# Kernel tuning notes

Hardware: AMD Instinct MI355X
Metric: run time of the kernel (lower is better)

The kernel has to match this reference:

```python
import jax, jax.numpy as jnp
import numpy as np

N = 4096
F_IN = 512
F_OUT = 64
H = 8
ALPHA = 0.2
NEG_BIG = -9e15


def setup_inputs() -> dict:
    key = jax.random.key(0)
    ks = jax.random.split(key, 7)
    h = jax.random.normal(ks[0], (N, F_IN), dtype=jnp.float32)
    mask = jax.random.randint(ks[1], (N, N), 0, 2, dtype=jnp.int32)
    # per-head linear W: weight [H, F_IN, F_OUT], bias [H, F_OUT] (xavier-ish scale)
    w_scale = 1.414 * np.sqrt(6.0 / (F_IN + F_OUT))
    W = jax.random.uniform(ks[2], (H, F_IN, F_OUT), dtype=jnp.float32, minval=-w_scale, maxval=w_scale)
    bW = jnp.zeros((H, F_OUT), dtype=jnp.float32)
    # attention linear A: [2*F_OUT, 1] split into a_l (acts on Wh_i) and a_r (acts on Wh_j)
    a_scale = 1.414 * np.sqrt(6.0 / (2 * F_OUT + 1))
    a_l = jax.random.uniform(ks[3], (H, F_OUT), dtype=jnp.float32, minval=-a_scale, maxval=a_scale)
    a_r = jax.random.uniform(ks[4], (H, F_OUT), dtype=jnp.float32, minval=-a_scale, maxval=a_scale)
    bA = jnp.zeros((H,), dtype=jnp.float32)
    return {"h": h, "mask": mask, "W": W, "bW": bW, "a_l": a_l, "a_r": a_r, "bA": bA}


def reference(h, mask, W, bW, a_l, a_r, bA):
    # Wh: [H, N, F_OUT]
    Wh = jnp.einsum('ni,hio->hno', h, W) + bW[:, None, :]
    # A([Wh_i ; Wh_j]) decomposed as outer sum: e[h,i,j] = a_l.Wh_i + a_r.Wh_j + bA
    el = jnp.einsum('hno,ho->hn', Wh, a_l)  # [H, N]
    er = jnp.einsum('hno,ho->hn', Wh, a_r)  # [H, N]
    e = el[:, :, None] + er[:, None, :] + bA[:, None, None]  # [H, N, N]
    e = jax.nn.leaky_relu(e, negative_slope=ALPHA)
    e = jnp.where(mask[None] > 0, e, NEG_BIG)
    a = jax.nn.softmax(e, axis=-1)  # softmax over neighbors j (dim=1 in torch)
    # dropout omitted (eval mode / deterministic reference)
    aWh = jnp.einsum('hij,hjo->hio', a, Wh)  # [H, N, F_OUT]
    out = jax.nn.elu(aWh)  # last=False
    # concat heads along feature dim -> [N, H*F_OUT]
    return jnp.transpose(out, (1, 0, 2)).reshape(N, H * F_OUT)
```

## Files before the change

### kernel.cpp

```cpp
#include <hip/hip_runtime.h>
#include <hip/hip_bf16.h>
#include <hip/hip_fp16.h>

#define NN 4096
#define FIN 512
#define FOUT 64
#define NH 8
#define ALPHA 0.2f
#define PSCALE 4096.0f

typedef unsigned int uint;
typedef unsigned short ushort;
typedef unsigned char uchar;
typedef unsigned long long ull;
typedef __attribute__((ext_vector_type(8))) short short8;
typedef __attribute__((ext_vector_type(8))) _Float16 half8;
typedef __attribute__((ext_vector_type(4))) float floatx4;
typedef __attribute__((ext_vector_type(4))) uint uintx4;
typedef __attribute__((ext_vector_type(2))) uint uintx2;

__device__ __forceinline__ float bf2f(ushort s) { return __uint_as_float(((uint)s) << 16); }
__device__ __forceinline__ ushort f2bf(float f) {
    uint u = __float_as_uint(f);
    u += 0x7fffu + ((u >> 16) & 1u);
    return (ushort)(u >> 16);
}
__device__ __forceinline__ ushort f2h(float f) {
    return __half_as_ushort(__float2half_rn(f));
}

__device__ __forceinline__ int detect_bf16(const ushort* __restrict__ hraw) {
    int lane = threadIdx.x & 63;
    float a = fabsf(bf2f(hraw[2 * lane]));
    ull bal = __ballot(a >= 1e-3f && a <= 100.0f);
    return __popcll(bal) >= 32;
}

#define PM_BLKS 8192
#define CV_BLKS 1024
#define TW_BLKS 32

__global__ __launch_bounds__(256) void prep_kernel(
    const int* __restrict__ mask, uchar* __restrict__ mb,
    const void* __restrict__ hraw, ushort* __restrict__ bh,
    const void* __restrict__ Wraw, ushort* __restrict__ WT)
{
    const int b = blockIdx.x, t = threadIdx.x;
    if (b < PM_BLKS) {
        size_t gid = (size_t)b * 256 + t;
        const int* p = mask + gid * 8;
        int4 aa = *(const int4*)p;
        int4 bb = *(const int4*)(p + 4);
        uint by = (uint)(aa.x > 0)        | ((uint)(aa.y > 0) << 1)
                | ((uint)(aa.z > 0) << 2) | ((uint)(aa.w > 0) << 3)
                | ((uint)(bb.x > 0) << 4) | ((uint)(bb.y > 0) << 5)
                | ((uint)(bb.z > 0) << 6) | ((uint)(bb.w > 0) << 7);
        mb[gid] = (uchar)by;
    } else if (b < PM_BLKS + CV_BLKS) {
        int isbf = detect_bf16((const ushort*)hraw);
        size_t e0 = ((size_t)(b - PM_BLKS) * 256 + t) * 8;
        if (isbf) {
            *(uint4*)(bh + e0) = *(const uint4*)((const ushort*)hraw + e0);
        } else {
            const float* s = (const float*)hraw + e0;
            float4 f0 = *(const float4*)s;
            float4 f1 = *(const float4*)(s + 4);
            uint4 o;
            o.x = (uint)f2bf(f0.x) | ((uint)f2bf(f0.y) << 16);
            o.y = (uint)f2bf(f0.z) | ((uint)f2bf(f0.w) << 16);
            o.z = (uint)f2bf(f1.x) | ((uint)f2bf(f1.y) << 16);
            o.w = (uint)f2bf(f1.z) | ((uint)f2bf(f1.w) << 16);
            *(uint4*)(bh + e0) = o;
        }
    } else {
        int isbf = detect_bf16((const ushort*)hraw);
        int b2 = b - PM_BLKS - CV_BLKS;
        int h = b2 >> 2, kq = b2 & 3;
        int o = t & 63, sub = t >> 6;
        int kbase = kq * 128 + sub * 32;
        uint pk[16];
#pragma unroll
        for (int kk = 0; kk < 32; kk += 2) {
            float v0, v1;
            size_t s0 = ((size_t)h * FIN + kbase + kk) * FOUT + o;
            size_t s1 = s0 + FOUT;
            if (isbf) { v0 = bf2f(((const ushort*)Wraw)[s0]); v1 = bf2f(((const ushort*)Wraw)[s1]); }
            else      { v0 = ((const float*)Wraw)[s0];        v1 = ((const float*)Wraw)[s1]; }
            pk[kk >> 1] = (uint)f2bf(v0) | ((uint)f2bf(v1) << 16);
        }
        ushort* dst = WT + ((size_t)h * FOUT + o) * FIN + kbase;
#pragma unroll
        for (int q = 0; q < 4; q++)
            *(uint4*)(dst + q * 8) = make_uint4(pk[q*4], pk[q*4+1], pk[q*4+2], pk[q*4+3]);
    }
}

__global__ __launch_bounds__(256) void khv_kernel(const float* __restrict__ er,
                                                  float* __restrict__ Kh,
                                                  ushort* __restrict__ vt,
                                                  ushort* __restrict__ zt) {
    __shared__ float red[256];
    int h = blockIdx.x >> 3, sl = blockIdx.x & 7, t = threadIdx.x;
    float m = -3.0e38f;
    for (int j = t; j < NN; j += 256) m = fmaxf(m, er[(size_t)h * NN + j]);
    red[t] = m;
    __syncthreads();
    for (int s = 128; s >= 1; s >>= 1) {
        if (t < s) red[t] = fmaxf(red[t], red[t + s]);
        __syncthreads();
    }
    float kh = red[0];
    if (t == 0 && sl == 0) Kh[h] = kh;
    int j = sl * 512 + t;
#pragma unroll
    for (int q = 0; q < 2; q++, j += 256) {
        float d = er[(size_t)h * NN + j] - kh;
        vt[(size_t)h * NN + j] = f2h(__expf(d));
        zt[(size_t)h * NN + j] = f2h(__expf(ALPHA * d));
    }
}

__global__ __launch_bounds__(256) void wh_kernel(
    const ushort* __restrict__ hmat, const ushort* __restrict__ WT,
    const void* __restrict__ bWr, const void* __restrict__ alr,
    const void* __restrict__ arr, const void* __restrict__ bAr,
    const ushort* __restrict__ hraw,
    ushort* __restrict__ WhT, float* __restrict__ el, float* __restrict__ er)
{
    __shared__ __align__(16) ushort sT[64][72];
    const int t = threadIdx.x, lane = t & 63, wid = t >> 6;
    const int head = blockIdx.y, rbase = blockIdx.x * 64;
    const int lm = lane & 15, lq = lane >> 4;

    floatx4 C[4];
#pragma unroll
    for (int cg = 0; cg < 4; cg++) C[cg] = (floatx4){0.f, 0.f, 0.f, 0.f};

    const ushort* Ap = hmat + (size_t)(rbase + wid * 16 + lm) * FIN + lq * 8;
    const ushort* Bp = WT + (size_t)head * FOUT * FIN + (size_t)lm * FIN + lq * 8;

#pragma unroll
    for (int kc = 0; kc < 16; kc++) {
        short8 a = *(const short8*)(Ap + kc * 32);
#pragma unroll
        for (int cg = 0; cg < 4; cg++) {
            short8 b = *(const short8*)(Bp + (size_t)cg * 16 * FIN + kc * 32);
            C[cg] = __builtin_amdgcn_mfma_f32_16x16x32_bf16(a, b, C[cg], 0, 0, 0);
        }
    }

    const int isbf = detect_bf16(hraw);
    float bA = isbf ? bf2f(((const ushort*)bAr)[head]) : ((const float*)bAr)[head];
    float pel[4] = {0.f, 0.f, 0.f, 0.f}, per[4] = {0.f, 0.f, 0.f, 0.f};
#pragma unroll
    for (int cg = 0; cg < 4; cg++) {
        int o = head * FOUT + cg * 16 + lm;
        float bw = isbf ? bf2f(((const ushort*)bWr)[o]) : ((const float*)bWr)[o];
        float av = isbf ? bf2f(((const ushort*)alr)[o]) : ((const float*)alr)[o];
        float rv = isbf ? bf2f(((const ushort*)arr)[o]) : ((const float*)arr)[o];
        ushort pk[4];
#pragma unroll
        for (int r = 0; r < 4; r++) {
            float v = C[cg][r] + bw;
            pel[r] += v * av;
            per[r] += v * rv;
            pk[r] = f2h(v);
        }
        ushort4 p4; p4.x = pk[0]; p4.y = pk[1]; p4.z = pk[2]; p4.w = pk[3];
        *(ushort4*)(&sT[cg * 16 + lm][wid * 16 + lq * 4]) = p4;
    }
#pragma unroll
    for (int off = 1; off < 16; off <<= 1) {
#pragma unroll
        for (int r = 0; r < 4; r++) {
            pel[r] += __shfl_xor(pel[r], off);
            per[r] += __shfl_xor(per[r], off);
        }
    }
    if (lm == 0) {
#pragma unroll
        for (int r = 0; r < 4; r++) {
            int row = rbase + wid * 16 + lq * 4 + r;
            el[(size_t)head * NN + row] = pel[r];
            er[(size_t)head * NN + row] = per[r] + bA;
        }
    }
    __syncthreads();
    {
        int o = t >> 2, ch = t & 3;
        uint4 v0 = *(const uint4*)(&sT[o][ch * 16]);
        uint4 v1 = *(const uint4*)(&sT[o][ch * 16 + 8]);
        ushort* d = WhT + ((size_t)head * FOUT + o) * NN + rbase + ch * 16;
        *(uint4*)d = v0;
        *(uint4*)(d + 8) = v1;
    }
}

__device__ __forceinline__ uint pkmul(uint a, uint b) {
    uint d; asm("v_pk_mul_f16 %0,%1,%2" : "=v"(d) : "v"(a), "v"(b)); return d;
}
__device__ __forceinline__ uint pkmax(uint a, uint b) {
    uint d; asm("v_pk_max_f16 %0,%1,%2" : "=v"(d) : "v"(a), "v"(b)); return d;
}
__device__ __forceinline__ uint pmask2(uint a) {
    uint b = a & 3u;
    return ((b | (b << 15)) & 0x10001u) * 0xFFFFu;
}
__device__ __forceinline__ half8 pgen8h(uintx4 vv, uintx4 zz, uint mby,
                                        uint uip, uint wip) {
    union { uintx4 u; half8 h; } c;
    c.u.x = pkmax(pkmul(uip, vv.x), pkmul(wip, zz.x)) & pmask2(mby);
    c.u.y = pkmax(pkmul(uip, vv.y), pkmul(wip, zz.y)) & pmask2(mby >> 2);
    c.u.z = pkmax(pkmul(uip, vv.z), pkmul(wip, zz.z)) & pmask2(mby >> 4);
    c.u.w = pkmax(pkmul(uip, vv.w), pkmul(wip, zz.w)) & pmask2(mby >> 6);
    return c.h;
}

#define KEEP(x) asm volatile("" : "+v"(x))

#define VZLOAD(S, j0) do {                                   \
    v##S##a = *(const uintx4*)(gvt + (j0) + sh8);            \
    v##S##b = *(const uintx4*)(gvt + (j0) + 32 + sh8);       \
    z##S##a = *(const uintx4*)(gzt + (j0) + sh8);            \
    z##S##b = *(const uintx4*)(gzt + (j0) + 32 + sh8);       \
} while (0)

__global__ __launch_bounds__(256, 2) void attn_kernel(
    const uchar* __restrict__ mb,
    const ushort* __restrict__ WhT,
    const float* __restrict__ el, const float* __restrict__ Kh,
    const ushort* __restrict__ vt, const ushort* __restrict__ zt,
    const ushort* __restrict__ hraw,
    void* __restrict__ outv)
{
    __shared__ __align__(16) ushort sB[2][64 * 72];

    const int t = threadIdx.x, lane = t & 63, wid = t >> 6;
    const int b = blockIdx.x;
    const int head = b & 7;
    const int ibase = (b >> 3) * 64;
    const int lm = lane & 15, lq = lane >> 4;
    const int sh8 = lq * 8;

    const float kh = Kh[head];
    const int row = ibase + wid * 16 + lm;
    const float x = el[(size_t)head * NN + row] + kh;
    const float Mi = fmaxf(x, ALPHA * x);
    const uint uip = (uint)f2h(PSCALE * __expf(x - Mi)) * 0x10001u;
    const uint wip = (uint)f2h(PSCALE * __expf(ALPHA * x - Mi)) * 0x10001u;

    const int so = t >> 2;
    const int sc = (t & 3) * 16;
    const ushort* gB = WhT + ((size_t)head * FOUT + so) * NN + sc;
    const ushort* gvt = vt + (size_t)head * NN;
    const ushort* gzt = zt + (size_t)head * NN;
    const uchar* mrow = mb + (size_t)row * 512;

    uintx4 rr0, rr1;
    uintx2 mk_s;

    auto gload = [&](int j0) {
        rr0 = *(const uintx4*)(gB + j0);
        rr1 = *(const uintx4*)(gB + j0 + 8);
        mk_s = *(const uintx2*)(mrow + (j0 >> 3));
    };
    auto lwrite = [&](int buf) {
        ushort* d = &sB[buf][so * 72 + sc];
        *(uintx4*)(d)     = rr0;
        *(uintx4*)(d + 8) = rr1;
    };

    uintx4 v0a, v0b, z0a, z0b;
    uintx4 v1a, v1b, z1a, z1b;

    const half8 onesh = {(_Float16)1.f, (_Float16)1.f, (_Float16)1.f, (_Float16)1.f,
                         (_Float16)1.f, (_Float16)1.f, (_Float16)1.f, (_Float16)1.f};
    floatx4 Z = {0.f, 0.f, 0.f, 0.f};
    floatx4 C0 = Z, C1 = Z, C2 = Z, C3 = Z, Cd = Z;

    auto compute = [&](int buf, uintx2 mk,
                       uintx4 vA, uintx4 vB, uintx4 zA, uintx4 zB) {
        uint m0 = mk.x >> sh8;
        uint m1 = mk.y >> sh8;
        half8 a0 = pgen8h(vA, zA, m0, uip, wip);
        half8 a1 = pgen8h(vB, zB, m1, uip, wip);
        const ushort* base = &sB[buf][0];
        half8 b00 = *(const half8*)(base + (0  + lm) * 72 + sh8);
        half8 b10 = *(const half8*)(base + (16 + lm) * 72 + sh8);
        half8 b20 = *(const half8*)(base + (32 + lm) * 72 + sh8);
        half8 b30 = *(const half8*)(base + (48 + lm) * 72 + sh8);
        Cd = __builtin_amdgcn_mfma_f32_16x16x32_f16(a0, onesh, Cd, 0, 0, 0);
        C0 = __builtin_amdgcn_mfma_f32_16x16x32_f16(a0, b00, C0, 0, 0, 0);
        C1 = __builtin_amdgcn_mfma_f32_16x16x32_f16(a0, b10, C1, 0, 0, 0);
        C2 = __builtin_amdgcn_mfma_f32_16x16x32_f16(a0, b20, C2, 0, 0, 0);
        C3 = __builtin_amdgcn_mfma_f32_16x16x32_f16(a0, b30, C3, 0, 0, 0);
        half8 b01 = *(const half8*)(base + (0  + lm) * 72 + 32 + sh8);
        half8 b11 = *(const half8*)(base + (16 + lm) * 72 + 32 + sh8);
        half8 b21 = *(const half8*)(base + (32 + lm) * 72 + 32 + sh8);
        half8 b31 = *(const half8*)(base + (48 + lm) * 72 + 32 + sh8);
        Cd = __builtin_amdgcn_mfma_f32_16x16x32_f16(a1, onesh, Cd, 0, 0, 0);
        C0 = __builtin_amdgcn_mfma_f32_16x16x32_f16(a1, b01, C0, 0, 0, 0);
        C1 = __builtin_amdgcn_mfma_f32_16x16x32_f16(a1, b11, C1, 0, 0, 0);
        C2 = __builtin_amdgcn_mfma_f32_16x16x32_f16(a1, b21, C2, 0, 0, 0);
        C3 = __builtin_amdgcn_mfma_f32_16x16x32_f16(a1, b31, C3, 0, 0, 0);
    };

    uintx2 mk0, mk1;
    gload(0);
    lwrite(0);
    mk0 = mk_s;
    gload(64);
    VZLOAD(0, 0);
    KEEP(rr0); KEEP(rr1); KEEP(mk_s);
    KEEP(v0a); KEEP(v0b); KEEP(z0a); KEEP(z0b);
    __syncthreads();

    for (int it = 0; it < 64; it += 2) {
        lwrite(1);
        mk1 = mk_s;
        gload(((it + 2) & 63) * 64);
        VZLOAD(1, (it + 1) * 64);
        compute(0, mk0, v0a, v0b, z0a, z0b);
        KEEP(v1a); KEEP(v1b); KEEP(z1a); KEEP(z1b);
        KEEP(rr0); KEEP(rr1); KEEP(mk_s);
        __syncthreads();
        lwrite(0);
        mk0 = mk_s;
        gload(((it + 3) & 63) * 64);
        VZLOAD(0, ((it + 2) & 63) * 64);
        compute(1, mk1, v1a, v1b, z1a, z1b);
        KEEP(v0a); KEEP(v0b); KEEP(z0a); KEEP(z0b);
        KEEP(rr0); KEEP(rr1); KEEP(mk_s);
        __syncthreads();
    }

    const int isbf = detect_bf16(hraw);
#pragma unroll
    for (int r = 0; r < 4; r++) {
        int orow = ibase + wid * 16 + lq * 4 + r;
        float inv = 1.f / Cd[r];
        float x0 = C0[r] * inv; x0 = (x0 > 0.f) ? x0 : __expf(x0) - 1.f;
        float x1 = C1[r] * inv; x1 = (x1 > 0.f) ? x1 : __expf(x1) - 1.f;
        float x2 = C2[r] * inv; x2 = (x2 > 0.f) ? x2 : __expf(x2) - 1.f;
        float x3 = C3[r] * inv; x3 = (x3 > 0.f) ? x3 : __expf(x3) - 1.f;
        size_t base = (size_t)orow * (NH * FOUT) + head * FOUT + lm;
        if (isbf) {
            ushort* o = (ushort*)outv;
            o[base + 0]  = f2bf(x0);
            o[base + 16] = f2bf(x1);
            o[base + 32] = f2bf(x2);
            o[base + 48] = f2bf(x3);
        } else {
            float* o = (float*)outv;
            o[base + 0]  = x0;
            o[base + 16] = x1;
            o[base + 32] = x2;
            o[base + 48] = x3;
        }
    }
}

extern "C" void kernel_launch(void* const* d_in, const int* in_sizes, int n_in,
                              void* d_out, int out_size, void* d_ws, size_t ws_size,
                              hipStream_t stream)
{
    const void* hraw = d_in[0];
    const int*  mask = (const int*)d_in[1];
    const void* Wraw = d_in[2];
    const void* bWr  = d_in[3];
    const void* alr  = d_in[4];
    const void* arr  = d_in[5];
    const void* bAr  = d_in[6];

    char* w = (char*)d_ws;
    ushort* bh   = (ushort*)w;                  w += (size_t)NN * FIN * 2;
    ushort* WT   = (ushort*)w;                  w += (size_t)NH * FOUT * FIN * 2;
    ushort* WhT  = (ushort*)w;                  w += (size_t)NH * FOUT * NN * 2;
    float*  el   = (float*)w;                   w += (size_t)NH * NN * 4;
    float*  er   = (float*)w;                   w += (size_t)NH * NN * 4;
    float*  Kh   = (float*)w;                   w += 64;
    ushort* vt   = (ushort*)w;                  w += (size_t)NH * NN * 4;
    ushort* zt   = (ushort*)w;                  w += (size_t)NH * NN * 4;
    uchar*  mb   = (uchar*)w;                   w += (size_t)NN * 512;

    prep_kernel<<<PM_BLKS + CV_BLKS + TW_BLKS, 256, 0, stream>>>(
        mask, mb, hraw, bh, Wraw, WT);
    wh_kernel<<<dim3(NN / 64, NH), 256, 0, stream>>>(bh, WT, bWr, alr, arr, bAr,
                                                     (const ushort*)hraw, WhT, el, er);
    khv_kernel<<<64, 256, 0, stream>>>(er, Kh, vt, zt);
    attn_kernel<<<NN / 64 * NH, 256, 0, stream>>>(mb, WhT, el, Kh, vt, zt,
                                                  (const ushort*)hraw, d_out);
}
```

Baseline: 195.9 us.

## Split attention block into row pairs and key halves with LDS merge

Each wave now computes 32 query rows instead of 16, so every B fragment read from LDS is reused by twice as many MFMAs. The key dimension is split across wave pairs, each streaming half of the keys through its own double-buffered LDS tile. Partial accumulators are merged through LDS at the end, before normalization and ELU. This doubles the accumulator registers per wave and adds a final merge barrier, which may lower occupancy.

```diff
diff --git a/kernel.cpp b/kernel.cpp
--- a/kernel.cpp
+++ b/kernel.cpp
@@ -233,9 +233,11 @@
     const ushort* __restrict__ hraw,
     void* __restrict__ outv)
 {
-    __shared__ __align__(16) ushort sB[2][64 * 72];
+    __shared__ __align__(16) ushort sB[2][2][64 * 72];
 
     const int t = threadIdx.x, lane = t & 63, wid = t >> 6;
+    const int rg = wid >> 1;
+    const int jh = wid & 1;
     const int b = blockIdx.x;
     const int head = b & 7;
     const int ibase = (b >> 3) * 64;
@@ -243,31 +245,43 @@
     const int sh8 = lq * 8;
 
     const float kh = Kh[head];
-    const int row = ibase + wid * 16 + lm;
-    const float x = el[(size_t)head * NN + row] + kh;
-    const float Mi = fmaxf(x, ALPHA * x);
-    const uint uip = (uint)f2h(PSCALE * __expf(x - Mi)) * 0x10001u;
-    const uint wip = (uint)f2h(PSCALE * __expf(ALPHA * x - Mi)) * 0x10001u;
-
-    const int so = t >> 2;
-    const int sc = (t & 3) * 16;
-    const ushort* gB = WhT + ((size_t)head * FOUT + so) * NN + sc;
-    const ushort* gvt = vt + (size_t)head * NN;
-    const ushort* gzt = zt + (size_t)head * NN;
-    const uchar* mrow = mb + (size_t)row * 512;
-
-    uintx4 rr0, rr1;
-    uintx2 mk_s;
+    const int rowa = ibase + rg * 32 + lm;
+    const float xa = el[(size_t)head * NN + rowa] + kh;
+    const float xb = el[(size_t)head * NN + rowa + 16] + kh;
+    const float Ma = fmaxf(xa, ALPHA * xa);
+    const float Mb = fmaxf(xb, ALPHA * xb);
+    const uint uipa = (uint)f2h(PSCALE * __expf(xa - Ma)) * 0x10001u;
+    const uint wipa = (uint)f2h(PSCALE * __expf(ALPHA * xa - Ma)) * 0x10001u;
+    const uint uipb = (uint)f2h(PSCALE * __expf(xb - Mb)) * 0x10001u;
+    const uint wipb = (uint)f2h(PSCALE * __expf(ALPHA * xb - Mb)) * 0x10001u;
+
+    const int jb = jh * 2048;
+    const int st = rg * 64 + lane;
+    const int so = st >> 1;
+    const int sc = (st & 1) * 32;
+    const ushort* gB = WhT + ((size_t)head * FOUT + so) * NN + jb + sc;
+    const ushort* gvt = vt + (size_t)head * NN + jb;
+    const ushort* gzt = zt + (size_t)head * NN + jb;
+    const uchar* mra = mb + (size_t)rowa * 512 + (jb >> 3);
+    const uchar* mrb = mra + 16 * 512;
+
+    uintx4 rr0, rr1, rr2, rr3;
+    uintx2 mka_s, mkb_s;
 
     auto gload = [&](int j0) {
         rr0 = *(const uintx4*)(gB + j0);
         rr1 = *(const uintx4*)(gB + j0 + 8);
-        mk_s = *(const uintx2*)(mrow + (j0 >> 3));
+        rr2 = *(const uintx4*)(gB + j0 + 16);
+        rr3 = *(const uintx4*)(gB + j0 + 24);
+        mka_s = *(const uintx2*)(mra + (j0 >> 3));
+        mkb_s = *(const uintx2*)(mrb + (j0 >> 3));
     };
     auto lwrite = [&](int buf) {
-        ushort* d = &sB[buf][so * 72 + sc];
-        *(uintx4*)(d)     = rr0;
-        *(uintx4*)(d + 8) = rr1;
+        ushort* d = &sB[jh][buf][so * 72 + sc];
+        *(uintx4*)(d)      = rr0;
+        *(uintx4*)(d + 8)  = rr1;
+        *(uintx4*)(d + 16) = rr2;
+        *(uintx4*)(d + 24) = rr3;
     };
 
     uintx4 v0a, v0b, z0a, z0b;
@@ -276,86 +290,136 @@
     const half8 onesh = {(_Float16)1.f, (_Float16)1.f, (_Float16)1.f, (_Float16)1.f,
                          (_Float16)1.f, (_Float16)1.f, (_Float16)1.f, (_Float16)1.f};
     floatx4 Z = {0.f, 0.f, 0.f, 0.f};
-    floatx4 C0 = Z, C1 = Z, C2 = Z, C3 = Z, Cd = Z;
-
-    auto compute = [&](int buf, uintx2 mk,
+    floatx4 C0 = Z, C1 = Z, C2 = Z, C3 = Z, Cd0 = Z;
+    floatx4 C4 = Z, C5 = Z, C6 = Z, C7 = Z, Cd1 = Z;
+
+    auto compute = [&](int buf, uintx2 mka, uintx2 mkb,
                        uintx4 vA, uintx4 vB, uintx4 zA, uintx4 zB) {
-        uint m0 = mk.x >> sh8;
-        uint m1 = mk.y >> sh8;
-        half8 a0 = pgen8h(vA, zA, m0, uip, wip);
-        half8 a1 = pgen8h(vB, zB, m1, uip, wip);
-        const ushort* base = &sB[buf][0];
+        uint m0a = mka.x >> sh8;
+        uint m1a = mka.y >> sh8;
+        uint m0b = mkb.x >> sh8;
+        uint m1b = mkb.y >> sh8;
+        half8 a0 = pgen8h(vA, zA, m0a, uipa, wipa);
+        half8 a1 = pgen8h(vB, zB, m1a, uipa, wipa);
+        half8 a2 = pgen8h(vA, zA, m0b, uipb, wipb);
+        half8 a3 = pgen8h(vB, zB, m1b, uipb, wipb);
+        const ushort* base = &sB[jh][buf][0];
         half8 b00 = *(const half8*)(base + (0  + lm) * 72 + sh8);
         half8 b10 = *(const half8*)(base + (16 + lm) * 72 + sh8);
         half8 b20 = *(const half8*)(base + (32 + lm) * 72 + sh8);
         half8 b30 = *(const half8*)(base + (48 + lm) * 72 + sh8);
-        Cd = __builtin_amdgcn_mfma_f32_16x16x32_f16(a0, onesh, Cd, 0, 0, 0);
+        Cd0 = __builtin_amdgcn_mfma_f32_16x16x32_f16(a0, onesh, Cd0, 0, 0, 0);
+        Cd1 = __builtin_amdgcn_mfma_f32_16x16x32_f16(a2, onesh, Cd1, 0, 0, 0);
         C0 = __builtin_amdgcn_mfma_f32_16x16x32_f16(a0, b00, C0, 0, 0, 0);
+        C4 = __builtin_amdgcn_mfma_f32_16x16x32_f16(a2, b00, C4, 0, 0, 0);
         C1 = __builtin_amdgcn_mfma_f32_16x16x32_f16(a0, b10, C1, 0, 0, 0);
+        C5 = __builtin_amdgcn_mfma_f32_16x16x32_f16(a2, b10, C5, 0, 0, 0);
         C2 = __builtin_amdgcn_mfma_f32_16x16x32_f16(a0, b20, C2, 0, 0, 0);
+        C6 = __builtin_amdgcn_mfma_f32_16x16x32_f16(a2, b20, C6, 0, 0, 0);
         C3 = __builtin_amdgcn_mfma_f32_16x16x32_f16(a0, b30, C3, 0, 0, 0);
+        C7 = __builtin_amdgcn_mfma_f32_16x16x32_f16(a2, b30, C7, 0, 0, 0);
         half8 b01 = *(const half8*)(base + (0  + lm) * 72 + 32 + sh8);
         half8 b11 = *(const half8*)(base + (16 + lm) * 72 + 32 + sh8);
         half8 b21 = *(const half8*)(base + (32 + lm) * 72 + 32 + sh8);
         half8 b31 = *(const half8*)(base + (48 + lm) * 72 + 32 + sh8);
-        Cd = __builtin_amdgcn_mfma_f32_16x16x32_f16(a1, onesh, Cd, 0, 0, 0);
+        Cd0 = __builtin_amdgcn_mfma_f32_16x16x32_f16(a1, onesh, Cd0, 0, 0, 0);
+        Cd1 = __builtin_amdgcn_mfma_f32_16x16x32_f16(a3, onesh, Cd1, 0, 0, 0);
         C0 = __builtin_amdgcn_mfma_f32_16x16x32_f16(a1, b01, C0, 0, 0, 0);
+        C4 = __builtin_amdgcn_mfma_f32_16x16x32_f16(a3, b01, C4, 0, 0, 0);
         C1 = __builtin_amdgcn_mfma_f32_16x16x32_f16(a1, b11, C1, 0, 0, 0);
+        C5 = __builtin_amdgcn_mfma_f32_16x16x32_f16(a3, b11, C5, 0, 0, 0);
         C2 = __builtin_amdgcn_mfma_f32_16x16x32_f16(a1, b21, C2, 0, 0, 0);
+        C6 = __builtin_amdgcn_mfma_f32_16x16x32_f16(a3, b21, C6, 0, 0, 0);
         C3 = __builtin_amdgcn_mfma_f32_16x16x32_f16(a1, b31, C3, 0, 0, 0);
+        C7 = __builtin_amdgcn_mfma_f32_16x16x32_f16(a3, b31, C7, 0, 0, 0);
     };
 
-    uintx2 mk0, mk1;
+    uintx2 mka0, mkb0, mka1, mkb1;
     gload(0);
     lwrite(0);
-    mk0 = mk_s;
+    mka0 = mka_s; mkb0 = mkb_s;
     gload(64);
     VZLOAD(0, 0);
-    KEEP(rr0); KEEP(rr1); KEEP(mk_s);
+    KEEP(rr0); KEEP(rr1); KEEP(rr2); KEEP(rr3);
     KEEP(v0a); KEEP(v0b); KEEP(z0a); KEEP(z0b);
     __syncthreads();
 
-    for (int it = 0; it < 64; it += 2) {
+    for (int it = 0; it < 32; it += 2) {
         lwrite(1);
-        mk1 = mk_s;
-        gload(((it + 2) & 63) * 64);
+        mka1 = mka_s; mkb1 = mkb_s;
+        gload(((it + 2) & 31) * 64);
         VZLOAD(1, (it + 1) * 64);
-        compute(0, mk0, v0a, v0b, z0a, z0b);
+        compute(0, mka0, mkb0, v0a, v0b, z0a, z0b);
         KEEP(v1a); KEEP(v1b); KEEP(z1a); KEEP(z1b);
-        KEEP(rr0); KEEP(rr1); KEEP(mk_s);
+        KEEP(rr0); KEEP(rr1); KEEP(rr2); KEEP(rr3);
         __syncthreads();
         lwrite(0);
-        mk0 = mk_s;
-        gload(((it + 3) & 63) * 64);
-        VZLOAD(0, ((it + 2) & 63) * 64);
-        compute(1, mk1, v1a, v1b, z1a, z1b);
+        mka0 = mka_s; mkb0 = mkb_s;
+        gload(((it + 3) & 31) * 64);
+        VZLOAD(0, ((it + 2) & 31) * 64);
+        compute(1, mka1, mkb1, v1a, v1b, z1a, z1b);
         KEEP(v0a); KEEP(v0b); KEEP(z0a); KEEP(z0b);
-        KEEP(rr0); KEEP(rr1); KEEP(mk_s);
+        KEEP(rr0); KEEP(rr1); KEEP(rr2); KEEP(rr3);
         __syncthreads();
     }
 
-    const int isbf = detect_bf16(hraw);
-#pragma unroll
-    for (int r = 0; r < 4; r++) {
-        int orow = ibase + wid * 16 + lq * 4 + r;
-        float inv = 1.f / Cd[r];
-        float x0 = C0[r] * inv; x0 = (x0 > 0.f) ? x0 : __expf(x0) - 1.f;
-        float x1 = C1[r] * inv; x1 = (x1 > 0.f) ? x1 : __expf(x1) - 1.f;
-        float x2 = C2[r] * inv; x2 = (x2 > 0.f) ? x2 : __expf(x2) - 1.f;
-        float x3 = C3[r] * inv; x3 = (x3 > 0.f) ? x3 : __expf(x3) - 1.f;
-        size_t base = (size_t)orow * (NH * FOUT) + head * FOUT + lm;
-        if (isbf) {
-            ushort* o = (ushort*)outv;
-            o[base + 0]  = f2bf(x0);
-            o[base + 16] = f2bf(x1);
-            o[base + 32] = f2bf(x2);
-            o[base + 48] = f2bf(x3);
-        } else {
-            float* o = (float*)outv;
-            o[base + 0]  = x0;
-            o[base + 16] = x1;
-            o[base + 32] = x2;
-            o[base + 48] = x3;
+    float* mg = (float*)&sB[0][0][0];
+    const int mi = (rg * 64 + lane) * 44;
+    if (jh == 1) {
+        float* p = &mg[mi];
+        *(floatx4*)(p + 0)  = C0;  *(floatx4*)(p + 4)  = C1;
+        *(floatx4*)(p + 8)  = C2;  *(floatx4*)(p + 12) = C3;
+        *(floatx4*)(p + 16) = C4;  *(floatx4*)(p + 20) = C5;
+        *(floatx4*)(p + 24) = C6;  *(floatx4*)(p + 28) = C7;
+        *(floatx4*)(p + 32) = Cd0; *(floatx4*)(p + 36) = Cd1;
+    }
+    __syncthreads();
+    if (jh == 0) {
+        const float* p = &mg[mi];
+        C0 += *(const floatx4*)(p + 0);   C1 += *(const floatx4*)(p + 4);
+        C2 += *(const floatx4*)(p + 8);   C3 += *(const floatx4*)(p + 12);
+        C4 += *(const floatx4*)(p + 16);  C5 += *(const floatx4*)(p + 20);
+        C6 += *(const floatx4*)(p + 24);  C7 += *(const floatx4*)(p + 28);
+        Cd0 += *(const floatx4*)(p + 32); Cd1 += *(const floatx4*)(p + 36);
+
+        const int isbf = detect_bf16(hraw);
+#pragma unroll
+        for (int r = 0; r < 4; r++) {
+            int ra = ibase + rg * 32 + lq * 4 + r;
+            int rb = ra + 16;
+            float inva = 1.f / Cd0[r];
+            float invb = 1.f / Cd1[r];
+            float x0 = C0[r] * inva; x0 = (x0 > 0.f) ? x0 : __expf(x0) - 1.f;
+            float x1 = C1[r] * inva; x1 = (x1 > 0.f) ? x1 : __expf(x1) - 1.f;
+            float x2 = C2[r] * inva; x2 = (x2 > 0.f) ? x2 : __expf(x2) - 1.f;
+            float x3 = C3[r] * inva; x3 = (x3 > 0.f) ? x3 : __expf(x3) - 1.f;
+            float y0 = C4[r] * invb; y0 = (y0 > 0.f) ? y0 : __expf(y0) - 1.f;
+            float y1 = C5[r] * invb; y1 = (y1 > 0.f) ? y1 : __expf(y1) - 1.f;
+            float y2 = C6[r] * invb; y2 = (y2 > 0.f) ? y2 : __expf(y2) - 1.f;
+            float y3 = C7[r] * invb; y3 = (y3 > 0.f) ? y3 : __expf(y3) - 1.f;
+            size_t basea = (size_t)ra * (NH * FOUT) + head * FOUT + lm;
+            size_t baseb = (size_t)rb * (NH * FOUT) + head * FOUT + lm;
+            if (isbf) {
+                ushort* o = (ushort*)outv;
+                o[basea + 0]  = f2bf(x0);
+                o[basea + 16] = f2bf(x1);
+                o[basea + 32] = f2bf(x2);
+                o[basea + 48] = f2bf(x3);
+                o[baseb + 0]  = f2bf(y0);
+                o[baseb + 16] = f2bf(y1);
+                o[baseb + 32] = f2bf(y2);
+                o[baseb + 48] = f2bf(y3);
+            } else {
+                float* o = (float*)outv;
+                o[basea + 0]  = x0;
+                o[basea + 16] = x1;
+                o[basea + 32] = x2;
+                o[basea + 48] = x3;
+                o[baseb + 0]  = y0;
+                o[baseb + 16] = y1;
+                o[baseb + 32] = y2;
+                o[baseb + 48] = y3;
+            }
         }
     }
 }
```

Result: faster. 180.2 us (-8.0%).
